# Optimization experiments

Measured on AMD Instinct MI355X. Metric: run time of the kernel, lower is better.

Reference implementation:

```python
import jax, jax.numpy as jnp
import numpy as np

D_MODEL = 512
NUM_HEADS = 8
HEAD_DIM = D_MODEL // NUM_HEADS  # 64


def setup_inputs() -> dict:
    key = jax.random.key(0)
    k_x, k_wqkv, k_bqkv, k_wout, k_bout = jax.random.split(key, 5)
    B, L = 30, 2048
    s_in = 1.0 / np.sqrt(D_MODEL)
    return {
        "x": jax.random.normal(k_x, (B, L, D_MODEL), dtype=jnp.float32),
        "w_qkv": jax.random.uniform(k_wqkv, (3 * D_MODEL, D_MODEL), minval=-s_in, maxval=s_in, dtype=jnp.float32),
        "b_qkv": jax.random.uniform(k_bqkv, (3 * D_MODEL,), minval=-s_in, maxval=s_in, dtype=jnp.float32),
        "w_out": jax.random.uniform(k_wout, (D_MODEL, D_MODEL), minval=-s_in, maxval=s_in, dtype=jnp.float32),
        "b_out": jax.random.uniform(k_bout, (D_MODEL,), minval=-s_in, maxval=s_in, dtype=jnp.float32),
    }


def reference(x, w_qkv, b_qkv, w_out, b_out):
    B, L, _ = x.shape
    # QKV projection: (B, L, 3*d_model)
    qkv = jnp.einsum("bld,ed->ble", x, w_qkv) + b_qkv
    # NOTE: source discards the permute, so layout stays (B, L, H, 3*head_dim)
    qkv = qkv.reshape(B, L, NUM_HEADS, 3 * HEAD_DIM)
    q, k, v = jnp.split(qkv, 3, axis=-1)  # each (B, L, H, head_dim)
    # Attention contracts head_dim -> (B, L, H, H): attention OVER HEADS, faithful to bug
    scores = jnp.einsum("blhd,blgd->blhg", q, k) / np.sqrt(HEAD_DIM)
    # mask=False in source adds 0 -> no-op
    attn = jax.nn.softmax(scores, axis=-1)
    val = jnp.einsum("blhg,blgd->blhd", attn, v).reshape(B, L, D_MODEL)
    out = jnp.einsum("bld,ed->ble", val, w_out) + b_out
    return out
```

## Files before the change

### kernel.cpp

```cpp
#include <hip/hip_runtime.h>
#include <hip/hip_bf16.h>
#include <stdint.h>

typedef short    s16x8  __attribute__((ext_vector_type(8)));
typedef __bf16   bf16x8 __attribute__((ext_vector_type(8)));
typedef float    f32x4  __attribute__((ext_vector_type(4)));

__device__ __forceinline__ unsigned short f2bf(float f) {
    union { float f; unsigned u; } v; v.f = f;
    unsigned r = v.u + 0x7FFFu + ((v.u >> 16) & 1u);
    return (unsigned short)(r >> 16);
}
__device__ __forceinline__ float bf2f(unsigned short s) {
    union { unsigned u; float f; } v; v.u = ((unsigned)s) << 16;
    return v.f;
}

__device__ __forceinline__ void gload16(const void* g, void* l) {
    __builtin_amdgcn_global_load_lds(
        (const __attribute__((address_space(1))) void*)(uintptr_t)g,
        (__attribute__((address_space(3))) void*)(uintptr_t)l,
        16, 0, 0);
}

__global__ __launch_bounds__(256) void cvt_bf16(const float* __restrict__ in,
                                                unsigned short* __restrict__ out,
                                                int n4) {
    int i = blockIdx.x * blockDim.x + threadIdx.x;
    int stride = gridDim.x * blockDim.x;
    for (; i < n4; i += stride) {
        const float4 v = *(const float4*)(in + (size_t)i * 4);
        ushort4 o;
        o.x = f2bf(v.x); o.y = f2bf(v.y); o.z = f2bf(v.z); o.w = f2bf(v.w);
        *(ushort4*)(out + (size_t)i * 4) = o;
    }
}

template<int K, bool OUT_BF16>
__global__ __launch_bounds__(512, 2) void gemm256(
        const unsigned short* __restrict__ A,
        const unsigned short* __restrict__ B,
        const float* __restrict__ bias,
        void* __restrict__ Cvoid,
        int M, int N, int ntn) {
    constexpr int BM = 256, BN = 256, BK = 32, NT = K / BK;
    __shared__ unsigned short As[2][BM * BK];
    __shared__ unsigned short Bs[2][BN * BK];
    const int tid  = threadIdx.x;
    const int lane = tid & 63;
    const int wv   = tid >> 6;
    const int nwg = (int)gridDim.x;
    const int wg  = ((int)blockIdx.x & 7) * (nwg >> 3) + ((int)blockIdx.x >> 3);
    const int bm  = wg / ntn;
    const int bn  = wg % ntn;
    const int wr  = (wv >> 2) * 128;
    const int wc  = (wv & 3) * 64;
    const int lr  = lane & 15;
    const int ls  = lane >> 4;

    const unsigned short* Ag = A + (size_t)bm * BM * K;
    const unsigned short* Bg = B + (size_t)bn * BN * K;

    auto stage = [&](const unsigned short* G, unsigned short* lds) {
        #pragma unroll
        for (int p = 0; p < 2; ++p) {
            const int c     = p * 512 + tid;
            const int row   = c >> 2;
            const int slot  = c & 3;
            const int gslot = slot ^ ((row >> 1) & 3);
            gload16(G + (size_t)row * K + gslot * 8, (char*)lds + c * 16);
        }
    };
    auto frag = [&](const unsigned short* lds, int row) -> bf16x8 {
        const int slot = ls ^ ((row >> 1) & 3);
        return *(const bf16x8*)((const char*)lds + row * (BK * 2) + slot * 16);
    };

    f32x4 acc[8][4] = {};

    stage(Ag, As[0]);
    stage(Bg, Bs[0]);

    #pragma unroll
    for (int t = 0; t < NT; ++t) {
        const int cur = t & 1;
        if (t + 1 < NT) {
            stage(Ag + (t + 1) * BK, As[cur ^ 1]);
            stage(Bg + (t + 1) * BK, Bs[cur ^ 1]);
            asm volatile("s_waitcnt vmcnt(4)" ::: "memory");
        } else {
            asm volatile("s_waitcnt vmcnt(0)" ::: "memory");
        }
        __builtin_amdgcn_s_barrier();

        bf16x8 a0[4], b0[4];
        #pragma unroll
        for (int m = 0; m < 4; ++m) a0[m] = frag(As[cur], wr + m * 16 + lr);
        #pragma unroll
        for (int n = 0; n < 4; ++n) b0[n] = frag(Bs[cur], wc + n * 16 + lr);
        __builtin_amdgcn_s_barrier();
        __builtin_amdgcn_s_setprio(1);
        #pragma unroll
        for (int m = 0; m < 4; ++m)
            #pragma unroll
            for (int n = 0; n < 4; ++n)
                acc[m][n] = __builtin_amdgcn_mfma_f32_16x16x32_bf16(
                    a0[m], b0[n], acc[m][n], 0, 0, 0);
        __builtin_amdgcn_s_setprio(0);
        __builtin_amdgcn_s_barrier();

        bf16x8 a1[4];
        #pragma unroll
        for (int m = 0; m < 4; ++m) a1[m] = frag(As[cur], wr + 64 + m * 16 + lr);
        __builtin_amdgcn_s_barrier();
        __builtin_amdgcn_s_setprio(1);
        #pragma unroll
        for (int m = 0; m < 4; ++m)
            #pragma unroll
            for (int n = 0; n < 4; ++n)
                acc[4 + m][n] = __builtin_amdgcn_mfma_f32_16x16x32_bf16(
                    a1[m], b0[n], acc[4 + m][n], 0, 0, 0);
        __builtin_amdgcn_s_setprio(0);
        __builtin_amdgcn_s_barrier();
    }

    const int r0 = bm * BM + wr + ls * 4;
    const int c0 = bn * BN + wc + lr;
    #pragma unroll
    for (int n = 0; n < 4; ++n) {
        const int gc = c0 + n * 16;
        const float bv = bias[gc];
        #pragma unroll
        for (int m = 0; m < 8; ++m) {
            #pragma unroll
            for (int j = 0; j < 4; ++j) {
                const int gr = r0 + m * 16 + j;
                const float v = acc[m][n][j] + bv;
                if constexpr (OUT_BF16)
                    ((unsigned short*)Cvoid)[(size_t)gr * N + gc] = f2bf(v);
                else
                    ((float*)Cvoid)[(size_t)gr * N + gc] = v;
            }
        }
    }
}

__global__ __launch_bounds__(256) void attn_heads(
        const unsigned short* __restrict__ qkv,
        unsigned short* __restrict__ val,
        int M) {
    const int t    = blockIdx.x * 4 + (threadIdx.x >> 6);
    const int lane = threadIdx.x & 63;
    const int h    = lane >> 3;
    const int c    = lane & 7;
    const unsigned short* base = qkv + (size_t)t * 1536;

    s16x8 q8 = *(const s16x8*)(base + h * 192 + c * 8);
    float qf[8];
    #pragma unroll
    for (int j = 0; j < 8; ++j) qf[j] = bf2f((unsigned short)q8[j]);

    float s[8];
    #pragma unroll
    for (int g = 0; g < 8; ++g) {
        s16x8 k8 = *(const s16x8*)(base + g * 192 + 64 + c * 8);
        float p = 0.f;
        #pragma unroll
        for (int j = 0; j < 8; ++j) p += qf[j] * bf2f((unsigned short)k8[j]);
        s[g] = p;
    }
    #pragma unroll
    for (int mask = 1; mask <= 4; mask <<= 1)
        #pragma unroll
        for (int g = 0; g < 8; ++g)
            s[g] += __shfl_xor(s[g], mask, 64);

    float mx = -1e30f;
    #pragma unroll
    for (int g = 0; g < 8; ++g) { s[g] *= 0.125f; mx = fmaxf(mx, s[g]); }
    float sum = 0.f;
    #pragma unroll
    for (int g = 0; g < 8; ++g) { s[g] = __expf(s[g] - mx); sum += s[g]; }
    const float inv = 1.f / sum;

    float acc[8] = {0.f,0.f,0.f,0.f,0.f,0.f,0.f,0.f};
    #pragma unroll
    for (int g = 0; g < 8; ++g) {
        s16x8 v8 = *(const s16x8*)(base + g * 192 + 128 + c * 8);
        const float ag = s[g] * inv;
        #pragma unroll
        for (int j = 0; j < 8; ++j) acc[j] += ag * bf2f((unsigned short)v8[j]);
    }
    s16x8 ov;
    #pragma unroll
    for (int j = 0; j < 8; ++j) ov[j] = (short)f2bf(acc[j]);
    *(s16x8*)(val + (size_t)t * 512 + h * 64 + c * 8) = ov;
}

extern "C" void kernel_launch(void* const* d_in, const int* in_sizes, int n_in,
                              void* d_out, int out_size, void* d_ws, size_t ws_size,
                              hipStream_t stream) {
    const float* x     = (const float*)d_in[0];
    const float* w_qkv = (const float*)d_in[1];
    const float* b_qkv = (const float*)d_in[2];
    const float* w_out = (const float*)d_in[3];
    const float* b_out = (const float*)d_in[4];
    float* out = (float*)d_out;

    const int DM = 512;
    const int M  = in_sizes[0] / DM;

    unsigned short* xb    = (unsigned short*)d_ws;
    unsigned short* wqkvb = xb + (size_t)M * DM;
    unsigned short* woutb = wqkvb + (size_t)3 * DM * DM;
    unsigned short* qkvb  = woutb + (size_t)DM * DM;
    unsigned short* valb  = xb;

    cvt_bf16<<<2048, 256, 0, stream>>>(x, xb, M * DM / 4);
    cvt_bf16<<<96,   256, 0, stream>>>(w_qkv, wqkvb, 3 * DM * DM / 4);
    cvt_bf16<<<32,   256, 0, stream>>>(w_out, woutb, DM * DM / 4);

    gemm256<512, true><<<dim3((M / 256) * (3 * DM / 256)), 512, 0, stream>>>(
        xb, wqkvb, b_qkv, qkvb, M, 3 * DM, 3 * DM / 256);

    attn_heads<<<M / 4, 256, 0, stream>>>(qkvb, valb, M);

    gemm256<512, false><<<dim3((M / 256) * (DM / 256)), 512, 0, stream>>>(
        valb, woutb, b_out, out, M, DM, DM / 256);
}
```

Measured before the change: 319.6 us.

## Deepen GEMM LDS pipeline to four buffers with three-stage prefetch

Moves the bf16 GEMM from double buffering to a 4-slot LDS ring with three tiles prefetched ahead. Each iteration now needs a single barrier, and each wave loads all A/B fragments before one block of MFMAs instead of two phases with several barriers. The aim is to hide global-load latency and cut synchronisation overhead. In exchange LDS use doubles to 128KB per block, which likely limits occupancy to one block per CU despite launch_bounds(512,2), and more fragment registers are live at once.

```diff
diff --git a/kernel.cpp b/kernel.cpp
--- a/kernel.cpp
+++ b/kernel.cpp
@@ -44,8 +44,8 @@
         void* __restrict__ Cvoid,
         int M, int N, int ntn) {
     constexpr int BM = 256, BN = 256, BK = 32, NT = K / BK;
-    __shared__ unsigned short As[2][BM * BK];
-    __shared__ unsigned short Bs[2][BN * BK];
+    __shared__ unsigned short As[4][BM * BK];
+    __shared__ unsigned short Bs[4][BN * BK];
     const int tid  = threadIdx.x;
     const int lane = tid & 63;
     const int wv   = tid >> 6;
@@ -61,14 +61,19 @@
     const unsigned short* Ag = A + (size_t)bm * BM * K;
     const unsigned short* Bg = B + (size_t)bn * BN * K;
 
-    auto stage = [&](const unsigned short* G, unsigned short* lds) {
+    auto stage = [&](int t) {
+        const unsigned short* GA = Ag + t * BK;
+        const unsigned short* GB = Bg + t * BK;
+        char* la = (char*)As[t & 3];
+        char* lb = (char*)Bs[t & 3];
         #pragma unroll
         for (int p = 0; p < 2; ++p) {
             const int c     = p * 512 + tid;
             const int row   = c >> 2;
             const int slot  = c & 3;
             const int gslot = slot ^ ((row >> 1) & 3);
-            gload16(G + (size_t)row * K + gslot * 8, (char*)lds + c * 16);
+            gload16(GA + (size_t)row * K + gslot * 8, la + c * 16);
+            gload16(GB + (size_t)row * K + gslot * 8, lb + c * 16);
         }
     };
     auto frag = [&](const unsigned short* lds, int row) -> bf16x8 {
@@ -78,50 +83,32 @@
 
     f32x4 acc[8][4] = {};
 
-    stage(Ag, As[0]);
-    stage(Bg, Bs[0]);
+    stage(0); stage(1); stage(2);
 
     #pragma unroll
     for (int t = 0; t < NT; ++t) {
-        const int cur = t & 1;
-        if (t + 1 < NT) {
-            stage(Ag + (t + 1) * BK, As[cur ^ 1]);
-            stage(Bg + (t + 1) * BK, Bs[cur ^ 1]);
-            asm volatile("s_waitcnt vmcnt(4)" ::: "memory");
-        } else {
-            asm volatile("s_waitcnt vmcnt(0)" ::: "memory");
-        }
+        if (t <= NT - 3)      asm volatile("s_waitcnt vmcnt(8)" ::: "memory");
+        else if (t == NT - 2) asm volatile("s_waitcnt vmcnt(4)" ::: "memory");
+        else                  asm volatile("s_waitcnt vmcnt(0)" ::: "memory");
         __builtin_amdgcn_s_barrier();
-
-        bf16x8 a0[4], b0[4];
-        #pragma unroll
-        for (int m = 0; m < 4; ++m) a0[m] = frag(As[cur], wr + m * 16 + lr);
-        #pragma unroll
-        for (int n = 0; n < 4; ++n) b0[n] = frag(Bs[cur], wc + n * 16 + lr);
-        __builtin_amdgcn_s_barrier();
+        if (t + 3 < NT) stage(t + 3);
+
+        const unsigned short* la = As[t & 3];
+        const unsigned short* lb = Bs[t & 3];
+        bf16x8 af[8], bfr[4];
+        #pragma unroll
+        for (int m = 0; m < 8; ++m) af[m] = frag(la, wr + m * 16 + lr);
+        #pragma unroll
+        for (int n = 0; n < 4; ++n) bfr[n] = frag(lb, wc + n * 16 + lr);
+
         __builtin_amdgcn_s_setprio(1);
         #pragma unroll
-        for (int m = 0; m < 4; ++m)
+        for (int m = 0; m < 8; ++m)
             #pragma unroll
             for (int n = 0; n < 4; ++n)
                 acc[m][n] = __builtin_amdgcn_mfma_f32_16x16x32_bf16(
-                    a0[m], b0[n], acc[m][n], 0, 0, 0);
+                    af[m], bfr[n], acc[m][n], 0, 0, 0);
         __builtin_amdgcn_s_setprio(0);
-        __builtin_amdgcn_s_barrier();
-
-        bf16x8 a1[4];
-        #pragma unroll
-        for (int m = 0; m < 4; ++m) a1[m] = frag(As[cur], wr + 64 + m * 16 + lr);
-        __builtin_amdgcn_s_barrier();
-        __builtin_amdgcn_s_setprio(1);
-        #pragma unroll
-        for (int m = 0; m < 4; ++m)
-            #pragma unroll
-            for (int n = 0; n < 4; ++n)
-                acc[4 + m][n] = __builtin_amdgcn_mfma_f32_16x16x32_bf16(
-                    a1[m], b0[n], acc[4 + m][n], 0, 0, 0);
-        __builtin_amdgcn_s_setprio(0);
-        __builtin_amdgcn_s_barrier();
     }
 
     const int r0 = bm * BM + wr + ls * 4;
```

Result: no change. 314.5 us (-1.6%).
